# Optimization experiments

Hardware: AMD Instinct MI355X
Metric: run time of the kernel (lower is better)

The kernel has to match this reference:

```python
import jax, jax.numpy as jnp
import numpy as np

N = 8          # regular representation size
C = 8          # in_channels
NV = 40000     # num vertices
MN = 32        # max neighbors
B = N          # basis sizes (reg-to-reg and each Taylor order)


def setup_inputs() -> dict:
    key = jax.random.key(0)
    ks = jax.random.split(key, 12)
    x = jax.random.normal(ks[0], (NV, C, N), dtype=jnp.float32)
    neighbors = jax.random.randint(ks[1], (NV, MN), 0, NV)
    mask = jax.random.bernoulli(ks[2], 0.8, (NV, MN))
    ptm = jax.random.normal(ks[3], (NV, MN, N, N), dtype=jnp.float32)
    rel_pos_u = jax.random.normal(ks[4], (NV, MN, 2), dtype=jnp.float32)
    s = 0.02
    return {
        "x": x,
        "neighbors": neighbors,
        "mask": mask,
        "parallel_transport_matrices": ptm,
        "rel_pos_u": rel_pos_u,
        "reg_to_reg_basis": jax.random.normal(ks[5], (B, N, N), dtype=jnp.float32),
        "query_coeffs": s * jax.random.normal(ks[6], (C, B), dtype=jnp.float32),
        "key_coeffs": s * jax.random.normal(ks[7], (C, B), dtype=jnp.float32),
        "value_basis_zero_order": jax.random.normal(ks[8], (B, N, N), dtype=jnp.float32),
        "value_basis_first_order": jax.random.normal(ks[9], (B, 2, N, N), dtype=jnp.float32),
        "value_basis_second_order": jax.random.normal(ks[10], (B, 3, N, N), dtype=jnp.float32),
        "value_zero_params": s * jax.random.normal(ks[11], (C, B), dtype=jnp.float32),
        "value_first_params": s * jax.random.normal(jax.random.fold_in(key, 100), (C, B), dtype=jnp.float32),
        "value_second_params": s * jax.random.normal(jax.random.fold_in(key, 101), (C, B), dtype=jnp.float32),
    }


def reference(x, neighbors, mask, parallel_transport_matrices, rel_pos_u,
              reg_to_reg_basis, query_coeffs, key_coeffs,
              value_basis_zero_order, value_basis_first_order, value_basis_second_order,
              value_zero_params, value_first_params, value_second_params):
    m = mask.astype(x.dtype)                                # [V,M]
    # neighbor gather + mask + parallel transport
    x_neigh = x[neighbors] * m[:, :, None, None]            # [V,M,C,N]
    f = jnp.einsum('vnij,vncj->vnci', parallel_transport_matrices, x_neigh)

    # Q/K per-channel reg-to-reg maps summed over channels
    WQ = jnp.einsum('cb,bij->cij', query_coeffs, reg_to_reg_basis)
    WK = jnp.einsum('cb,bij->cij', key_coeffs, reg_to_reg_basis)
    Q = jnp.einsum('cij,vcj->vi', WQ, x)                    # [V,N]
    K = jnp.einsum('cij,vncj->vni', WK, f)                  # [V,M,N]

    # ReLU attention score, mean over N, masked, normalized over neighbors
    score = jnp.mean(jax.nn.relu(Q[:, None, :] + K), axis=-1)
    score = jnp.where(mask, score, jnp.zeros((), x.dtype))  # [V,M]
    denom = jnp.clip(jnp.sum(score, axis=-1), 1e-8, None)
    attention = score / denom[:, None]

    # Taylor-expanded value map (fused einsums; no [V,M,C,N,N] intermediate)
    u0 = rel_pos_u[..., 0]
    u1 = rel_pos_u[..., 1]
    u_quad = jnp.stack([u0 * u0, 2.0 * u0 * u1, u1 * u1], axis=-1)  # [V,M,3]
    W0 = jnp.einsum('cb,bij->cij', value_zero_params, value_basis_zero_order)
    values = jnp.einsum('cij,vncj->vnci', W0, f)
    values += jnp.einsum('cb,boij,vno,vncj->vnci', value_first_params,
                         value_basis_first_order, rel_pos_u, f)
    values += jnp.einsum('cb,boij,vno,vncj->vnci', value_second_params,
                         value_basis_second_order, u_quad, f)

    return jnp.einsum('vn,vnci->vci', attention, values)    # [V,C,N]
```

## Files before the change

### kernel.cpp

```cpp
#include <hip/hip_runtime.h>

#define NVERT 40000


typedef __fp16 hf2 __attribute__((ext_vector_type(2)));

__device__ __forceinline__ void wave_lds_fence() {
  asm volatile("s_waitcnt lgkmcnt(0)" ::: "memory");
}

__device__ __forceinline__ hf2 pk_h2(float a, float b) {
  return __builtin_amdgcn_cvt_pkrtz(a, b);
}
__device__ __forceinline__ unsigned int h2u(hf2 h) {
  unsigned int u; __builtin_memcpy(&u, &h, 4); return u;
}
__device__ __forceinline__ hf2 uh2(unsigned int u) {
  hf2 h; __builtin_memcpy(&h, &u, 4); return h;
}
__device__ __forceinline__ float fdot2(hf2 a, hf2 b, float c) {
#if __has_builtin(__builtin_amdgcn_fdot2)
  return __builtin_amdgcn_fdot2(a, b, c, false);
#else
  return (float)a.x * (float)b.x + (float)a.y * (float)b.y + c;
#endif
}

__device__ __forceinline__ float rs8(const float v[8], int c) {
  float snd, kp, s0, s1, s2, s3, t0, t1;
  snd = (c & 1) ? v[0] : v[1]; kp = (c & 1) ? v[1] : v[0]; s0 = kp + __shfl_xor(snd, 1);
  snd = (c & 1) ? v[2] : v[3]; kp = (c & 1) ? v[3] : v[2]; s1 = kp + __shfl_xor(snd, 1);
  snd = (c & 1) ? v[4] : v[5]; kp = (c & 1) ? v[5] : v[4]; s2 = kp + __shfl_xor(snd, 1);
  snd = (c & 1) ? v[6] : v[7]; kp = (c & 1) ? v[7] : v[6]; s3 = kp + __shfl_xor(snd, 1);
  snd = (c & 2) ? s0 : s1;     kp = (c & 2) ? s1 : s0;     t0 = kp + __shfl_xor(snd, 2);
  snd = (c & 2) ? s2 : s3;     kp = (c & 2) ? s3 : s2;     t1 = kp + __shfl_xor(snd, 2);
  snd = (c & 4) ? t0 : t1;     kp = (c & 4) ? t1 : t0;     return kp + __shfl_xor(snd, 4);
}

__device__ __forceinline__ float rs8n(const float v[8], int n8) {
  float snd, kp, s0, s1, s2, s3, t0, t1;
  snd = (n8 & 1) ? v[0] : v[1]; kp = (n8 & 1) ? v[1] : v[0]; s0 = kp + __shfl_xor(snd, 8);
  snd = (n8 & 1) ? v[2] : v[3]; kp = (n8 & 1) ? v[3] : v[2]; s1 = kp + __shfl_xor(snd, 8);
  snd = (n8 & 1) ? v[4] : v[5]; kp = (n8 & 1) ? v[5] : v[4]; s2 = kp + __shfl_xor(snd, 8);
  snd = (n8 & 1) ? v[6] : v[7]; kp = (n8 & 1) ? v[7] : v[6]; s3 = kp + __shfl_xor(snd, 8);
  snd = (n8 & 2) ? s0 : s1;     kp = (n8 & 2) ? s1 : s0;     t0 = kp + __shfl_xor(snd, 16);
  snd = (n8 & 2) ? s2 : s3;     kp = (n8 & 2) ? s3 : s2;     t1 = kp + __shfl_xor(snd, 16);
  snd = (n8 & 4) ? t0 : t1;     kp = (n8 & 4) ? t1 : t0;     return kp + __shfl_xor(snd, 32);
}

__global__ __launch_bounds__(256, 2)
void ge_attn(const float* __restrict__ x,
             const int* __restrict__ nbr,
             const void* __restrict__ maskp,
             const float* __restrict__ ptm,
             const float* __restrict__ rpu,
             const float* __restrict__ rbasis,
             const float* __restrict__ qcoef,
             const float* __restrict__ kcoef,
             const float* __restrict__ vb0,
             const float* __restrict__ vb1,
             const float* __restrict__ vb2,
             const float* __restrict__ vp0,
             const float* __restrict__ vp1,
             const float* __restrict__ vp2,
             float* __restrict__ out)
{
  __shared__ __align__(16) unsigned int sWqkH[512];
  __shared__ __align__(16) unsigned int sWvH[1536];
  __shared__ __align__(16) unsigned short sF[4][2048];
  __shared__ float sU[4][64];
  __shared__ int sFlagB, sFlagF;

  const int tid = threadIdx.x;
  if (tid == 0) { sFlagB = 0; sFlagF = 0; }
  __syncthreads();

  {
    const unsigned int* mw = (const unsigned int*)maskp;
    int b0 = 0, b1 = 0;
#pragma unroll
    for (int t = 0; t < 8; ++t) {
      const unsigned int w = mw[tid + (t << 8)];
      b1 |= (w == 0x3F800000u) ? 1 : 0;
      b0 |= (w > 1u && w != 0x3F800000u) ? 1 : 0;
    }
    if (b0) sFlagB = 1;
    if (b1) sFlagF = 1;
  }

  for (int r = tid; r < 512; r += 256) {
    const int m = r >> 6;
    const int cc = (r >> 3) & 7;
    const int ii = r & 7;
    const float* par; const float* bas; int ospan, oo;
    switch (m) {
      case 0:  par = qcoef; bas = rbasis; ospan = 1; oo = 0; break;
      case 1:  par = kcoef; bas = rbasis; ospan = 1; oo = 0; break;
      case 2:  par = vp0;   bas = vb0;    ospan = 1; oo = 0; break;
      case 3:  par = vp1;   bas = vb1;    ospan = 2; oo = 0; break;
      case 4:  par = vp1;   bas = vb1;    ospan = 2; oo = 1; break;
      case 5:  par = vp2;   bas = vb2;    ospan = 3; oo = 0; break;
      case 6:  par = vp2;   bas = vb2;    ospan = 3; oo = 1; break;
      default: par = vp2;   bas = vb2;    ospan = 3; oo = 2; break;
    }
    float acc[8] = {0,0,0,0,0,0,0,0};
#pragma unroll
    for (int b = 0; b < 8; ++b) {
      const float cf = par[cc*8 + b];
      const float* row = bas + (((b*ospan + oo)*8 + ii) << 3);
#pragma unroll
      for (int j = 0; j < 8; ++j) acc[j] += cf * row[j];
    }
    if (m < 2) {
      unsigned int* dst = sWqkH + (m << 8) + (((ii << 3) + cc) << 2);
      uint4 w;
      w.x = h2u(pk_h2(acc[0], acc[1]));
      w.y = h2u(pk_h2(acc[2], acc[3]));
      w.z = h2u(pk_h2(acc[4], acc[5]));
      w.w = h2u(pk_h2(acc[6], acc[7]));
      *(uint4*)dst = w;
    } else {
      unsigned short* dstH = (unsigned short*)sWvH;
      const int o = m - 2;
#pragma unroll
      for (int j = 0; j < 8; ++j) {
        unsigned int hu = h2u(pk_h2(acc[j], acc[j]));
        dstH[(((o << 8) + ((ii >> 1) << 6) + (cc << 3) + j) << 1) | (ii & 1)] =
            (unsigned short)(hu & 0xFFFFu);
      }
    }
  }
  __syncthreads();

  const int mode = sFlagB ? 1 : (sFlagF ? 2 : 0);

  const int wv   = tid >> 6;
  const int lane = tid & 63;
  const int n8   = lane >> 3;
  const int c    = lane & 7;
  const int v    = (blockIdx.x << 2) + wv;
  unsigned short* sFw = sF[wv];
  float* sUw = sU[wv];

  int nbv[4];
  int mkbits = 0;
#pragma unroll
  for (int p = 0; p < 4; ++p) {
    const int mi = (v << 5) + (p << 3) + n8;
    nbv[p] = nbr[mi];
    int mk;
    if (mode == 1)      mk = ((const unsigned char*)maskp)[mi] != 0;
    else if (mode == 2) mk = ((((const unsigned int*)maskp)[mi]) & 0x7FFFFFFFu) != 0u;
    else                mk = ((const int*)maskp)[mi] != 0;
    mkbits |= (mk << p);
  }
  if (c < 4) {
    const int mi = (v << 5) + (c << 3) + n8;
    const float2 uu = *(const float2*)(rpu + ((size_t)mi << 1));
    *(float2*)&sUw[((c << 3) + n8) << 1] = uu;
  }

  float Q1;
  {
    const float* xq = x + ((size_t)v << 6) + (c << 3);
    const float4 qa = *(const float4*)xq;
    const float4 qb = *(const float4*)(xq + 4);
    hf2 xh0 = pk_h2(qa.x, qa.y), xh1 = pk_h2(qa.z, qa.w);
    hf2 xh2 = pk_h2(qb.x, qb.y), xh3 = pk_h2(qb.z, qb.w);
    float qp[8];
#pragma unroll
    for (int i = 0; i < 8; ++i) {
      const uint4 w = *(const uint4*)&sWqkH[((i << 3) + c) << 2];
      qp[i] = fdot2(uh2(w.w), xh3, fdot2(uh2(w.z), xh2,
              fdot2(uh2(w.y), xh1, fdot2(uh2(w.x), xh0, 0.0f))));
    }
    Q1 = rs8(qp, c);
  }

  {
    const float4* p4 = (const float4*)(ptm + (size_t)v * 2048);
#pragma unroll
    for (int t = 0; t < 8; ++t) {
      const int g = lane + (t << 6);
      const float4 val = p4[g];
      const int n  = g >> 4;
      const int ii = (g >> 1) & 7;
      const int hh = g & 1;
      const int unit = (n << 3) | (ii ^ (n & 7));
      *(uint2*)&sFw[(unit << 3) + (hh << 2)] =
          make_uint2(h2u(pk_h2(val.x, val.y)), h2u(pk_h2(val.z, val.w)));
    }
  }

  wave_lds_fence();

  float s[4];
  const float* xb0 = x + ((size_t)nbv[0] << 6) + (c << 3);
  float4 xa = *(const float4*)xb0;
  float4 xc = *(const float4*)(xb0 + 4);
#pragma unroll
  for (int p = 0; p < 4; ++p) {
    float4 xan, xcn;
    if (p < 3) {
      const float* xbn = x + ((size_t)nbv[p + 1] << 6) + (c << 3);
      xan = *(const float4*)xbn;
      xcn = *(const float4*)(xbn + 4);
    }
    hf2 xh0 = pk_h2(xa.x, xa.y), xh1 = pk_h2(xa.z, xa.w);
    hf2 xh2 = pk_h2(xc.x, xc.y), xh3 = pk_h2(xc.z, xc.w);
    const int rowb = ((p << 3) + n8) << 3;
    hf2 fh0, fh1, fh2, fh3;
    float fprev;
#pragma unroll
    for (int i = 0; i < 8; ++i) {
      const uint4 r = *(const uint4*)&sFw[(rowb | (i ^ n8)) << 3];
      const float fcur =
          fdot2(uh2(r.w), xh3, fdot2(uh2(r.z), xh2,
          fdot2(uh2(r.y), xh1, fdot2(uh2(r.x), xh0, 0.0f))));
      if ((i & 1) == 0) {
        fprev = fcur;
      } else {
        const hf2 pk = pk_h2(fprev, fcur);
        if (i == 1) fh0 = pk;
        else if (i == 3) fh1 = pk;
        else if (i == 5) fh2 = pk;
        else fh3 = pk;
      }
    }
    float kp[8];
#pragma unroll
    for (int i = 0; i < 8; ++i) {
      const uint4 w = *(const uint4*)&sWqkH[256 + (((i << 3) + c) << 2)];
      kp[i] = fdot2(uh2(w.w), fh3, fdot2(uh2(w.z), fh2,
              fdot2(uh2(w.y), fh1, fdot2(uh2(w.x), fh0, 0.0f))));
    }
    const float K1 = rs8(kp, c);
    float sc = fmaxf(Q1 + K1, 0.0f);
    sc += __shfl_xor(sc, 1);
    sc += __shfl_xor(sc, 2);
    sc += __shfl_xor(sc, 4);
    s[p] = ((mkbits >> p) & 1) ? sc * 0.125f : 0.0f;

    *(uint4*)&sFw[(rowb | (c ^ n8)) << 3] =
        make_uint4(h2u(fh0), h2u(fh1), h2u(fh2), h2u(fh3));

    if (p < 3) { xa = xan; xc = xcn; }
  }

  float dt = s[0] + s[1] + s[2] + s[3];
  dt += __shfl_xor(dt, 8);
  dt += __shfl_xor(dt, 16);
  dt += __shfl_xor(dt, 32);
  const float rden = 1.0f / fmaxf(dt, 1e-8f);
#pragma unroll
  for (int p = 0; p < 4; ++p) s[p] *= rden;

  wave_lds_fence();

  hf2 zp[4];
#pragma unroll
  for (int q = 0; q < 4; ++q) zp[q] = uh2(0u);
#pragma unroll
  for (int hlf = 0; hlf < 2; ++hlf) {
    hf2 tp0[4], tp1[4], tp2[4];
#pragma unroll
    for (int q = 0; q < 4; ++q) { tp0[q] = uh2(0u); tp1[q] = uh2(0u); tp2[q] = uh2(0u); }
#pragma unroll
    for (int p = 0; p < 4; ++p) {
      const uint4 r = *(const uint4*)&sFw[(((((p << 3) + n8) << 3)) | (c ^ n8)) << 3];
      const hf2 f0 = uh2(r.x), f1 = uh2(r.y), f2 = uh2(r.z), f3 = uh2(r.w);
      const float2 uu = *(const float2*)&sUw[((p << 3) + n8) << 1];
      const float a = s[p];
      float cf0, cf1, cf2;
      if (hlf == 0) { cf0 = a;                  cf1 = a * uu.x;               cf2 = a * uu.y; }
      else          { cf0 = a * uu.x * uu.x;    cf1 = 2.0f * a * uu.x * uu.y; cf2 = a * uu.y * uu.y; }
      const hf2 ch0 = pk_h2(cf0, cf0), ch1 = pk_h2(cf1, cf1), ch2 = pk_h2(cf2, cf2);
      tp0[0] += ch0 * f0; tp0[1] += ch0 * f1; tp0[2] += ch0 * f2; tp0[3] += ch0 * f3;
      tp1[0] += ch1 * f0; tp1[1] += ch1 * f1; tp1[2] += ch1 * f2; tp1[3] += ch1 * f3;
      tp2[0] += ch2 * f0; tp2[1] += ch2 * f1; tp2[2] += ch2 * f2; tp2[3] += ch2 * f3;
    }
    float t0[8], t1[8], t2[8];
#pragma unroll
    for (int q = 0; q < 4; ++q) {
      t0[2*q] = (float)tp0[q].x; t0[2*q + 1] = (float)tp0[q].y;
      t1[2*q] = (float)tp1[q].x; t1[2*q + 1] = (float)tp1[q].y;
      t2[2*q] = (float)tp2[q].x; t2[2*q + 1] = (float)tp2[q].y;
    }
    const float h0 = rs8n(t0, n8);
    const float h1 = rs8n(t1, n8);
    const float h2 = rs8n(t2, n8);
    const hf2 hh0 = pk_h2(h0, h0), hh1 = pk_h2(h1, h1), hh2 = pk_h2(h2, h2);
    const int ob = hlf * 3;
    const int wbase = (c << 3) + n8;
#pragma unroll
    for (int q = 0; q < 4; ++q) {
      zp[q] += hh0 * uh2(sWvH[((ob + 0) << 8) + (q << 6) + wbase])
             + hh1 * uh2(sWvH[((ob + 1) << 8) + (q << 6) + wbase])
             + hh2 * uh2(sWvH[((ob + 2) << 8) + (q << 6) + wbase]);
    }
  }
  float zacc[8];
#pragma unroll
  for (int q = 0; q < 4; ++q) {
    zacc[2*q]     = (float)zp[q].x;
    zacc[2*q + 1] = (float)zp[q].y;
  }
  const float outv = rs8n(zacc, n8);
  out[((size_t)v << 6) + (c << 3) + n8] = outv;
}

extern "C" void kernel_launch(void* const* d_in, const int* in_sizes, int n_in,
                              void* d_out, int out_size, void* d_ws, size_t ws_size,
                              hipStream_t stream) {
  const float* x   = (const float*)d_in[0];
  const int*   nb  = (const int*)d_in[1];
  const void*  msk = d_in[2];
  const float* ptm = (const float*)d_in[3];
  const float* rpu = (const float*)d_in[4];
  const float* rb  = (const float*)d_in[5];
  const float* qc  = (const float*)d_in[6];
  const float* kc  = (const float*)d_in[7];
  const float* vb0 = (const float*)d_in[8];
  const float* vb1 = (const float*)d_in[9];
  const float* vb2 = (const float*)d_in[10];
  const float* vp0 = (const float*)d_in[11];
  const float* vp1 = (const float*)d_in[12];
  const float* vp2 = (const float*)d_in[13];
  (void)in_sizes; (void)n_in; (void)out_size; (void)d_ws; (void)ws_size;

  ge_attn<<<NVERT / 4, 256, 0, stream>>>(x, nb, msk, ptm, rpu, rb, qc, kc,
                                         vb0, vb1, vb2, vp0, vp1, vp2,
                                         (float*)d_out);
}
```

Measured before the change: 139.0 us.

## Accumulate Taylor value partials in registers inside the score loop

Folds the value-side Taylor accumulation into the per-neighbor score loop, so the transported features stay in registers and are no longer written to and read back from LDS. The relative-position data is now loaded straight into registers per neighbor instead of being staged in shared memory. Attention normalization moves after the neighbor reduction as a single multiply by the reciprocal denominator. In exchange, six packed-half accumulator arrays stay live across the loop, which raises register pressure and may lower occupancy. Accumulating unnormalized scores in fp16 also carries some overflow and precision risk.

```diff
diff --git a/kernel.cpp b/kernel.cpp
--- a/kernel.cpp
+++ b/kernel.cpp
@@ -68,7 +68,6 @@
   __shared__ __align__(16) unsigned int sWqkH[512];
   __shared__ __align__(16) unsigned int sWvH[1536];
   __shared__ __align__(16) unsigned short sF[4][2048];
-  __shared__ float sU[4][64];
   __shared__ int sFlagB, sFlagF;
 
   const int tid = threadIdx.x;
@@ -140,24 +139,21 @@
   const int c    = lane & 7;
   const int v    = (blockIdx.x << 2) + wv;
   unsigned short* sFw = sF[wv];
-  float* sUw = sU[wv];
 
   int nbv[4];
+  float u0[4], u1[4];
   int mkbits = 0;
 #pragma unroll
   for (int p = 0; p < 4; ++p) {
     const int mi = (v << 5) + (p << 3) + n8;
     nbv[p] = nbr[mi];
+    const float2 uu = *(const float2*)(rpu + ((size_t)mi << 1));
+    u0[p] = uu.x; u1[p] = uu.y;
     int mk;
     if (mode == 1)      mk = ((const unsigned char*)maskp)[mi] != 0;
     else if (mode == 2) mk = ((((const unsigned int*)maskp)[mi]) & 0x7FFFFFFFu) != 0u;
     else                mk = ((const int*)maskp)[mi] != 0;
     mkbits |= (mk << p);
-  }
-  if (c < 4) {
-    const int mi = (v << 5) + (c << 3) + n8;
-    const float2 uu = *(const float2*)(rpu + ((size_t)mi << 1));
-    *(float2*)&sUw[((c << 3) + n8) << 1] = uu;
   }
 
   float Q1;
@@ -193,6 +189,13 @@
   }
 
   wave_lds_fence();
+
+  hf2 tp0[4], tp1[4], tp2[4], tp3[4], tp4[4], tp5[4];
+#pragma unroll
+  for (int q = 0; q < 4; ++q) {
+    tp0[q] = uh2(0u); tp1[q] = uh2(0u); tp2[q] = uh2(0u);
+    tp3[q] = uh2(0u); tp4[q] = uh2(0u); tp5[q] = uh2(0u);
+  }
 
   float s[4];
   const float* xb0 = x + ((size_t)nbv[0] << 6) + (c << 3);
@@ -239,10 +242,19 @@
     sc += __shfl_xor(sc, 1);
     sc += __shfl_xor(sc, 2);
     sc += __shfl_xor(sc, 4);
-    s[p] = ((mkbits >> p) & 1) ? sc * 0.125f : 0.0f;
-
-    *(uint4*)&sFw[(rowb | (c ^ n8)) << 3] =
-        make_uint4(h2u(fh0), h2u(fh1), h2u(fh2), h2u(fh3));
+    const float sp = ((mkbits >> p) & 1) ? sc * 0.125f : 0.0f;
+    s[p] = sp;
+
+    const float c1 = sp * u0[p], c2 = sp * u1[p];
+    const float c3 = c1 * u0[p], c4 = 2.0f * c1 * u1[p], c5 = c2 * u1[p];
+    const hf2 ch0 = pk_h2(sp, sp), ch1 = pk_h2(c1, c1), ch2 = pk_h2(c2, c2);
+    const hf2 ch3 = pk_h2(c3, c3), ch4 = pk_h2(c4, c4), ch5 = pk_h2(c5, c5);
+    tp0[0] += ch0*fh0; tp0[1] += ch0*fh1; tp0[2] += ch0*fh2; tp0[3] += ch0*fh3;
+    tp1[0] += ch1*fh0; tp1[1] += ch1*fh1; tp1[2] += ch1*fh2; tp1[3] += ch1*fh3;
+    tp2[0] += ch2*fh0; tp2[1] += ch2*fh1; tp2[2] += ch2*fh2; tp2[3] += ch2*fh3;
+    tp3[0] += ch3*fh0; tp3[1] += ch3*fh1; tp3[2] += ch3*fh2; tp3[3] += ch3*fh3;
+    tp4[0] += ch4*fh0; tp4[1] += ch4*fh1; tp4[2] += ch4*fh2; tp4[3] += ch4*fh3;
+    tp5[0] += ch5*fh0; tp5[1] += ch5*fh1; tp5[2] += ch5*fh2; tp5[3] += ch5*fh3;
 
     if (p < 3) { xa = xan; xc = xcn; }
   }
@@ -252,53 +264,37 @@
   dt += __shfl_xor(dt, 16);
   dt += __shfl_xor(dt, 32);
   const float rden = 1.0f / fmaxf(dt, 1e-8f);
-#pragma unroll
-  for (int p = 0; p < 4; ++p) s[p] *= rden;
-
-  wave_lds_fence();
 
   hf2 zp[4];
 #pragma unroll
   for (int q = 0; q < 4; ++q) zp[q] = uh2(0u);
-#pragma unroll
-  for (int hlf = 0; hlf < 2; ++hlf) {
-    hf2 tp0[4], tp1[4], tp2[4];
-#pragma unroll
-    for (int q = 0; q < 4; ++q) { tp0[q] = uh2(0u); tp1[q] = uh2(0u); tp2[q] = uh2(0u); }
-#pragma unroll
-    for (int p = 0; p < 4; ++p) {
-      const uint4 r = *(const uint4*)&sFw[(((((p << 3) + n8) << 3)) | (c ^ n8)) << 3];
-      const hf2 f0 = uh2(r.x), f1 = uh2(r.y), f2 = uh2(r.z), f3 = uh2(r.w);
-      const float2 uu = *(const float2*)&sUw[((p << 3) + n8) << 1];
-      const float a = s[p];
-      float cf0, cf1, cf2;
-      if (hlf == 0) { cf0 = a;                  cf1 = a * uu.x;               cf2 = a * uu.y; }
-      else          { cf0 = a * uu.x * uu.x;    cf1 = 2.0f * a * uu.x * uu.y; cf2 = a * uu.y * uu.y; }
-      const hf2 ch0 = pk_h2(cf0, cf0), ch1 = pk_h2(cf1, cf1), ch2 = pk_h2(cf2, cf2);
-      tp0[0] += ch0 * f0; tp0[1] += ch0 * f1; tp0[2] += ch0 * f2; tp0[3] += ch0 * f3;
-      tp1[0] += ch1 * f0; tp1[1] += ch1 * f1; tp1[2] += ch1 * f2; tp1[3] += ch1 * f3;
-      tp2[0] += ch2 * f0; tp2[1] += ch2 * f1; tp2[2] += ch2 * f2; tp2[3] += ch2 * f3;
-    }
-    float t0[8], t1[8], t2[8];
-#pragma unroll
-    for (int q = 0; q < 4; ++q) {
-      t0[2*q] = (float)tp0[q].x; t0[2*q + 1] = (float)tp0[q].y;
-      t1[2*q] = (float)tp1[q].x; t1[2*q + 1] = (float)tp1[q].y;
-      t2[2*q] = (float)tp2[q].x; t2[2*q + 1] = (float)tp2[q].y;
-    }
-    const float h0 = rs8n(t0, n8);
-    const float h1 = rs8n(t1, n8);
-    const float h2 = rs8n(t2, n8);
-    const hf2 hh0 = pk_h2(h0, h0), hh1 = pk_h2(h1, h1), hh2 = pk_h2(h2, h2);
-    const int ob = hlf * 3;
-    const int wbase = (c << 3) + n8;
-#pragma unroll
-    for (int q = 0; q < 4; ++q) {
-      zp[q] += hh0 * uh2(sWvH[((ob + 0) << 8) + (q << 6) + wbase])
-             + hh1 * uh2(sWvH[((ob + 1) << 8) + (q << 6) + wbase])
-             + hh2 * uh2(sWvH[((ob + 2) << 8) + (q << 6) + wbase]);
-    }
-  }
+  const int wbase = (c << 3) + n8;
+
+#define VAL_HALF(TPA, TPB, TPC, OB)                                          \
+  {                                                                          \
+    float t0[8], t1[8], t2[8];                                               \
+    _Pragma("unroll")                                                        \
+    for (int q = 0; q < 4; ++q) {                                            \
+      t0[2*q] = (float)TPA[q].x; t0[2*q+1] = (float)TPA[q].y;                \
+      t1[2*q] = (float)TPB[q].x; t1[2*q+1] = (float)TPB[q].y;                \
+      t2[2*q] = (float)TPC[q].x; t2[2*q+1] = (float)TPC[q].y;                \
+    }                                                                        \
+    const float h0 = rden * rs8n(t0, n8);                                    \
+    const float h1 = rden * rs8n(t1, n8);                                    \
+    const float h2 = rden * rs8n(t2, n8);                                    \
+    const hf2 hh0 = pk_h2(h0, h0), hh1 = pk_h2(h1, h1), hh2 = pk_h2(h2, h2); \
+    _Pragma("unroll")                                                        \
+    for (int q = 0; q < 4; ++q) {                                            \
+      zp[q] += hh0 * uh2(sWvH[((OB + 0) << 8) + (q << 6) + wbase])           \
+             + hh1 * uh2(sWvH[((OB + 1) << 8) + (q << 6) + wbase])           \
+             + hh2 * uh2(sWvH[((OB + 2) << 8) + (q << 6) + wbase]);          \
+    }                                                                        \
+  }
+
+  VAL_HALF(tp0, tp1, tp2, 0)
+  VAL_HALF(tp3, tp4, tp5, 3)
+#undef VAL_HALF
+
   float zacc[8];
 #pragma unroll
   for (int q = 0; q < 4; ++q) {
```

Measured after the change: 144.7 us. 1.04x slower.
